# Kernel optimization log

Hardware: AMD Instinct MI355X
Metric: run time of the kernel (lower is better)

## Reference

```python
import jax, jax.numpy as jnp
import numpy as np

# Config: AydinConfig(hidden_dim=1024, intermediate_dim=2048, num_experts=8, top_k=2)
E, H, I, K = 8, 1024, 2048, 2
B, S = 4, 2048


def setup_inputs() -> dict:
    key = jax.random.key(0)
    k1, k2, k3, k4 = jax.random.split(key, 4)
    x = jax.random.normal(k1, (B, S, H), dtype=jnp.float32)
    # nn.Linear(H, E, bias=False): weight shape (E, H), default init ~ U(-1/sqrt(H), 1/sqrt(H))
    router_w = jax.random.uniform(k2, (E, H), dtype=jnp.float32,
                                  minval=-1.0, maxval=1.0) / np.sqrt(H).astype(np.float32)
    # normal init, std=0.02 (reset_parameters)
    w13 = jax.random.normal(k3, (E, H, 2 * I), dtype=jnp.float32) * 0.02
    w2 = jax.random.normal(k4, (E, I, H), dtype=jnp.float32) * 0.02
    return {"x": x, "router_w": router_w, "w13": w13, "w2": w2}


def reference(x, router_w, w13, w2):
    # Router: logits (B,S,E) -> softmax -> top-k with renormalized weights
    logits = jnp.einsum('bsh,eh->bse', x, router_w)
    probs = jax.nn.softmax(logits, axis=-1)
    weights, indices = jax.lax.top_k(probs, K)            # (B,S,K)
    weights = weights / (weights.sum(axis=-1, keepdims=True) + 1e-6)
    # Expert SwiGLU, computed densely over all experts then gathered.
    # Same math as the torch per-token weight gather, but avoids the
    # (B,S,K,H,2I) gathered-weight blowup.
    h13 = jnp.einsum('bsh,ehi->bsei', x, w13)             # (B,S,E,2I)
    gate, up = jnp.split(h13, 2, axis=-1)                 # (B,S,E,I) each
    h = jax.nn.silu(gate) * up
    y = jnp.einsum('bsei,eih->bseh', h, w2)               # (B,S,E,H)
    # Gather top-k expert outputs and combine with routing weights
    y_sel = jnp.take_along_axis(y, indices[..., None], axis=2)  # (B,S,K,H)
    return (y_sel * weights[..., None]).sum(axis=2)       # (B,S,H)
```

## Files before the change

kernel.cpp:

```cpp
#include <hip/hip_runtime.h>
#include <hip/hip_bf16.h>
#include <math.h>

#define NEXP 8
#define HD 1024
#define ID 2048
#define NTOK 8192
#define NROWS 16384

typedef __bf16 bf16_t;
typedef __bf16 bf16x8 __attribute__((ext_vector_type(8)));
typedef float f32x4 __attribute__((ext_vector_type(4)));

#define BK1 64
#define BK2 128
#define MAXT1 72
#define MAXT2 136

__device__ __forceinline__ void gl16(const void* g, void* l) {
    __builtin_amdgcn_global_load_lds(
        (const __attribute__((address_space(1))) unsigned int*)g,
        (__attribute__((address_space(3))) unsigned int*)l, 16, 0, 0);
}

__global__ __launch_bounds__(256)
void router_kernel(const float* __restrict__ x, const float* __restrict__ rw,
                   bf16_t* __restrict__ xb, int* __restrict__ topk_idx,
                   float* __restrict__ topk_w)
{
    const int t = blockIdx.x;
    const int tid = threadIdx.x;
    const float4 xv = ((const float4*)(x + (size_t)t * HD))[tid];
    float acc[NEXP];
#pragma unroll
    for (int e = 0; e < NEXP; ++e) {
        const float4 w4 = ((const float4*)(rw + e * HD))[tid];
        acc[e] = xv.x * w4.x + xv.y * w4.y + xv.z * w4.z + xv.w * w4.w;
    }
    bf16_t tmp[4] = {(bf16_t)xv.x, (bf16_t)xv.y, (bf16_t)xv.z, (bf16_t)xv.w};
    *(uint2*)(xb + (size_t)t * HD + tid * 4) = *(const uint2*)tmp;

    __shared__ float red[4][NEXP];
    const int lane = tid & 63, wv = tid >> 6;
#pragma unroll
    for (int e = 0; e < NEXP; ++e) {
        float v = acc[e];
#pragma unroll
        for (int off = 32; off >= 1; off >>= 1) v += __shfl_down(v, off, 64);
        if (lane == 0) red[wv][e] = v;
    }
    __syncthreads();
    if (tid == 0) {
        float lg[NEXP], mx = -1e30f;
#pragma unroll
        for (int e = 0; e < NEXP; ++e) {
            lg[e] = red[0][e] + red[1][e] + red[2][e] + red[3][e];
            mx = fmaxf(mx, lg[e]);
        }
        float p[NEXP], s = 0.f;
#pragma unroll
        for (int e = 0; e < NEXP; ++e) { p[e] = __expf(lg[e] - mx); s += p[e]; }
        const float inv = 1.f / s;
#pragma unroll
        for (int e = 0; e < NEXP; ++e) p[e] *= inv;
        int i0 = 0; float p0 = p[0];
#pragma unroll
        for (int e = 1; e < NEXP; ++e) if (p[e] > p0) { p0 = p[e]; i0 = e; }
        int i1 = -1; float p1 = -1.f;
#pragma unroll
        for (int e = 0; e < NEXP; ++e) if (e != i0 && p[e] > p1) { p1 = p[e]; i1 = e; }
        const float d = 1.f / (p0 + p1 + 1e-6f);
        topk_idx[t * 2 + 0] = i0; topk_idx[t * 2 + 1] = i1;
        topk_w[t * 2 + 0] = p0 * d; topk_w[t * 2 + 1] = p1 * d;
    }
}

__global__ __launch_bounds__(256)
void count_kernel(const int* __restrict__ topk_idx, int* __restrict__ counts)
{
    __shared__ int lc[NEXP];
    const int tid = threadIdx.x;
    if (tid < NEXP) lc[tid] = 0;
    __syncthreads();
    const int t = blockIdx.x * 256 + tid;
    atomicAdd(&lc[topk_idx[t * 2 + 0]], 1);
    atomicAdd(&lc[topk_idx[t * 2 + 1]], 1);
    __syncthreads();
    if (tid < NEXP) atomicAdd(&counts[tid], lc[tid]);
}

__global__ void scan_kernel(const int* __restrict__ counts, int* __restrict__ offsets,
                            int* __restrict__ cursor,
                            unsigned* __restrict__ map256, unsigned* __restrict__ map128)
{
    __shared__ int tb2[NEXP + 1], tb1[NEXP + 1];
    if (threadIdx.x == 0) {
        int s = 0, t2 = 0, t1 = 0;
        for (int e = 0; e < NEXP; ++e) {
            offsets[e] = s; cursor[e] = s; s += counts[e];
            tb2[e] = t2; t2 += (counts[e] + 255) >> 8;
            tb1[e] = t1; t1 += (counts[e] + 127) >> 7;
        }
        tb2[NEXP] = t2; tb1[NEXP] = t1;
    }
    __syncthreads();
    for (int i = threadIdx.x; i < MAXT1; i += 64) {
        unsigned v = 0xFFFFFFFFu;
#pragma unroll
        for (int e = 0; e < NEXP; ++e)
            if (i >= tb2[e] && i < tb2[e + 1]) v = ((unsigned)e << 16) | (unsigned)(i - tb2[e]);
        map256[i] = v;
    }
    for (int i = threadIdx.x; i < MAXT2; i += 64) {
        unsigned v = 0xFFFFFFFFu;
#pragma unroll
        for (int e = 0; e < NEXP; ++e)
            if (i >= tb1[e] && i < tb1[e + 1]) v = ((unsigned)e << 16) | (unsigned)(i - tb1[e]);
        map128[i] = v;
    }
}

__global__ __launch_bounds__(256)
void scatter_kernel(const int* __restrict__ topk_idx, const float* __restrict__ topk_w,
                    int* __restrict__ cursor, int* __restrict__ token_list,
                    float* __restrict__ row_w, int* __restrict__ row_pos)
{
    __shared__ int lc[NEXP], gbase[NEXP];
    const int tid = threadIdx.x;
    if (tid < NEXP) lc[tid] = 0;
    __syncthreads();
    const int t = blockIdx.x * 256 + tid;
    const int e0 = topk_idx[t * 2 + 0], e1 = topk_idx[t * 2 + 1];
    const int lp0 = atomicAdd(&lc[e0], 1);
    const int lp1 = atomicAdd(&lc[e1], 1);
    __syncthreads();
    if (tid < NEXP) gbase[tid] = atomicAdd(&cursor[tid], lc[tid]);
    __syncthreads();
    const int p0 = gbase[e0] + lp0, p1 = gbase[e1] + lp1;
    token_list[p0] = t; row_w[p0] = topk_w[t * 2 + 0]; row_pos[t * 2 + 0] = p0;
    token_list[p1] = t; row_w[p1] = topk_w[t * 2 + 1]; row_pos[t * 2 + 1] = p1;
}

__global__ __launch_bounds__(256)
void precast_kernel(const float* __restrict__ src, bf16_t* __restrict__ dst,
                    int K, int N)
{
    const int e = blockIdx.z;
    src += (size_t)e * K * N;
    dst += (size_t)e * K * N;
    const int n0 = blockIdx.x * 64, k0 = blockIdx.y * 64;
    __shared__ float tile[64][65];
    const int tid = threadIdx.x;
    const int tx = (tid & 15) * 4, ty = tid >> 4;
#pragma unroll
    for (int p = 0; p < 4; ++p) {
        const float4 v = *(const float4*)(src + (size_t)(k0 + ty + p * 16) * N + n0 + tx);
        tile[ty + p * 16][tx + 0] = v.x;
        tile[ty + p * 16][tx + 1] = v.y;
        tile[ty + p * 16][tx + 2] = v.z;
        tile[ty + p * 16][tx + 3] = v.w;
    }
    __syncthreads();
    const int n = tid >> 2, kc = (tid & 3) * 16;
    bf16_t outv[16];
#pragma unroll
    for (int j = 0; j < 16; ++j) outv[j] = (bf16_t)tile[kc + j][n];
    bf16_t* d = dst + (size_t)(n0 + n) * K + k0 + kc;
    *(uint4*)d = *(uint4*)outv;
    *(uint4*)(d + 8) = *((uint4*)outv + 1);
}

__global__ __launch_bounds__(512)
void gemm1_kernel(const bf16_t* __restrict__ xb, const bf16_t* __restrict__ w13b,
                  const int* __restrict__ offsets, const int* __restrict__ counts,
                  const int* __restrict__ token_list,
                  const unsigned* __restrict__ tile_map, bf16_t* __restrict__ hbuf)
{
    unsigned id = blockIdx.y * 32u + blockIdx.x;
    id = (id & 7u) * 288u + (id >> 3);
    const unsigned tm = tile_map[id >> 5];
    if (tm == 0xFFFFFFFFu) return;
    const int e = (int)(tm >> 16), mt = (int)(tm & 0xFFFFu);
    const int rows = counts[e];
    const int row_base = offsets[e];
    const int r0 = mt * 256;
    const int n0 = (int)(id & 31u) * 64;

    __shared__ alignas(16) bf16_t As[256][64];
    __shared__ alignas(16) bf16_t Bg[64][64];
    __shared__ alignas(16) bf16_t Bu[64][64];

    const int tid = threadIdx.x;
    const int lane = tid & 63;
    const int wv = tid >> 6;
    const int wr = wv >> 1, wc = wv & 1;
    const int ln15 = lane & 15, q = lane >> 4;
    const int x7 = ln15 & 7;
    const int c0 = ((q ^ x7)) * 8;
    const int c1 = c0 ^ 32;

    const int srow = tid >> 3;
    const int scol = ((tid & 7) ^ ((tid >> 3) & 7)) * 8;
    const bf16_t* ap[4];
#pragma unroll
    for (int p = 0; p < 4; ++p) {
        int gr = row_base + r0 + p * 64 + srow;
        if (gr > NROWS - 1) gr = NROWS - 1;
        ap[p] = xb + (size_t)token_list[gr] * HD + scol;
    }
    const bf16_t* wb = w13b + (size_t)e * HD * (2 * ID);
    const bf16_t* bgp = wb + (size_t)(n0 + srow) * HD + scol;
    const bf16_t* bup = wb + (size_t)(ID + n0 + srow) * HD + scol;
    bf16_t* const d_bg = &Bg[0][0] + tid * 8;
    bf16_t* const d_bu = &Bu[0][0] + tid * 8;

    f32x4 accG[4][2], accU[4][2];
#pragma unroll
    for (int i = 0; i < 4; ++i)
#pragma unroll
        for (int j = 0; j < 2; ++j)
#pragma unroll
            for (int c = 0; c < 4; ++c) { accG[i][j][c] = 0.f; accU[i][j][c] = 0.f; }

    for (int k0 = 0; k0 < HD; k0 += BK1) {
#pragma unroll
        for (int p = 0; p < 4; ++p) {
            gl16(ap[p], &As[0][0] + (p * 512 + tid) * 8);
            ap[p] += BK1;
        }
        gl16(bgp, d_bg); gl16(bup, d_bu);
        bgp += BK1; bup += BK1;
        __syncthreads();

#pragma unroll
        for (int kk = 0; kk < 2; ++kk) {
            const int cc = kk ? c1 : c0;
            bf16x8 af[4], bgf[2], buf_[2];
#pragma unroll
            for (int i = 0; i < 4; ++i)
                af[i] = *(const bf16x8*)&As[wr * 64 + i * 16 + ln15][cc];
#pragma unroll
            for (int j = 0; j < 2; ++j) {
                bgf[j]  = *(const bf16x8*)&Bg[wc * 32 + j * 16 + ln15][cc];
                buf_[j] = *(const bf16x8*)&Bu[wc * 32 + j * 16 + ln15][cc];
            }
#pragma unroll
            for (int i = 0; i < 4; ++i)
#pragma unroll
                for (int j = 0; j < 2; ++j) {
                    accG[i][j] = __builtin_amdgcn_mfma_f32_16x16x32_bf16(af[i], bgf[j], accG[i][j], 0, 0, 0);
                    accU[i][j] = __builtin_amdgcn_mfma_f32_16x16x32_bf16(af[i], buf_[j], accU[i][j], 0, 0, 0);
                }
        }
        __syncthreads();
    }

#pragma unroll
    for (int i = 0; i < 4; ++i) {
#pragma unroll
        for (int reg = 0; reg < 4; ++reg) {
            const int rr = wr * 64 + i * 16 + q * 4 + reg;
            if (r0 + rr < rows) {
                bf16_t* dst = hbuf + (size_t)(row_base + r0 + rr) * ID + n0 + wc * 32 + ln15;
#pragma unroll
                for (int j = 0; j < 2; ++j) {
                    const float g = accG[i][j][reg], u = accU[i][j][reg];
                    dst[j * 16] = (bf16_t)((g / (1.f + __expf(-g))) * u);
                }
            }
        }
    }
}

__global__ __launch_bounds__(512)
void gemm2_kernel(const bf16_t* __restrict__ hbuf, const bf16_t* __restrict__ w2b,
                  const int* __restrict__ offsets, const int* __restrict__ counts,
                  const float* __restrict__ row_w,
                  const unsigned* __restrict__ tile_map, float* __restrict__ ybuf)
{
    const unsigned tm = tile_map[blockIdx.y];
    if (tm == 0xFFFFFFFFu) return;
    const int e = (int)(tm >> 16), mt = (int)(tm & 0xFFFFu);
    const int rows = counts[e];
    const int row_base = offsets[e];
    const int r0 = mt * 128;
    const int n0 = blockIdx.x * 128;

    __shared__ alignas(16) bf16_t As[128][128];
    __shared__ alignas(16) bf16_t Bs[128][128];
    __shared__ float rww_s[128];

    const int tid = threadIdx.x;
    if (tid < 128) {
        int gr = row_base + r0 + tid; if (gr > NROWS - 1) gr = NROWS - 1;
        rww_s[tid] = row_w[gr];
    }
    const int lane = tid & 63;
    const int wv = tid >> 6;
    const int wr = wv >> 1, wc = wv & 1;
    const int ln15 = lane & 15, q = lane >> 4;

    const int srow = tid >> 4;
    const int scol = ((tid & 15) ^ ((tid >> 4) & 15)) * 8;
    const bf16_t* ap[4];
    const bf16_t* bp[4];
    const bf16_t* w2e = w2b + (size_t)e * ID * HD;
#pragma unroll
    for (int p = 0; p < 4; ++p) {
        int gr = row_base + r0 + p * 32 + srow;
        if (gr > NROWS - 1) gr = NROWS - 1;
        ap[p] = hbuf + (size_t)gr * ID + scol;
        bp[p] = w2e + (size_t)(n0 + p * 32 + srow) * ID + scol;
    }

    f32x4 acc[2][4];
#pragma unroll
    for (int i = 0; i < 2; ++i)
#pragma unroll
        for (int j = 0; j < 4; ++j)
#pragma unroll
            for (int c = 0; c < 4; ++c) acc[i][j][c] = 0.f;

    for (int k0 = 0; k0 < ID; k0 += BK2) {
#pragma unroll
        for (int p = 0; p < 4; ++p) {
            gl16(ap[p], &As[0][0] + (p * 512 + tid) * 8);
            gl16(bp[p], &Bs[0][0] + (p * 512 + tid) * 8);
            ap[p] += BK2; bp[p] += BK2;
        }
        __syncthreads();

#pragma unroll
        for (int kk = 0; kk < 4; ++kk) {
            const int cc = ((kk * 4 + q) ^ ln15) * 8;
            bf16x8 af[2], bf_[4];
#pragma unroll
            for (int i = 0; i < 2; ++i)
                af[i] = *(const bf16x8*)&As[wr * 32 + i * 16 + ln15][cc];
#pragma unroll
            for (int j = 0; j < 4; ++j)
                bf_[j] = *(const bf16x8*)&Bs[wc * 64 + j * 16 + ln15][cc];
#pragma unroll
            for (int i = 0; i < 2; ++i)
#pragma unroll
                for (int j = 0; j < 4; ++j)
                    acc[i][j] = __builtin_amdgcn_mfma_f32_16x16x32_bf16(af[i], bf_[j], acc[i][j], 0, 0, 0);
        }
        __syncthreads();
    }

#pragma unroll
    for (int i = 0; i < 2; ++i) {
#pragma unroll
        for (int reg = 0; reg < 4; ++reg) {
            const int rr = wr * 32 + i * 16 + q * 4 + reg;
            if (r0 + rr < rows) {
                const float w = rww_s[rr];
                float* dst = ybuf + (size_t)(row_base + r0 + rr) * HD + n0 + wc * 64 + ln15;
#pragma unroll
                for (int j = 0; j < 4; ++j)
                    dst[j * 16] = acc[i][j][reg] * w;
            }
        }
    }
}

__global__ __launch_bounds__(256)
void combine_kernel(const float* __restrict__ ybuf, const int* __restrict__ row_pos,
                    float* __restrict__ out)
{
    const int t = blockIdx.x;
    const int p0 = row_pos[t * 2 + 0], p1 = row_pos[t * 2 + 1];
    const float4 a = ((const float4*)(ybuf + (size_t)p0 * HD))[threadIdx.x];
    const float4 b = ((const float4*)(ybuf + (size_t)p1 * HD))[threadIdx.x];
    float4 o; o.x = a.x + b.x; o.y = a.y + b.y; o.z = a.z + b.z; o.w = a.w + b.w;
    ((float4*)(out + (size_t)t * HD))[threadIdx.x] = o;
}

extern "C" void kernel_launch(void* const* d_in, const int* in_sizes, int n_in,
                              void* d_out, int out_size, void* d_ws, size_t ws_size,
                              hipStream_t stream) {
    const float* x   = (const float*)d_in[0];
    const float* rw  = (const float*)d_in[1];
    const float* w13 = (const float*)d_in[2];
    const float* w2  = (const float*)d_in[3];
    float* out = (float*)d_out;

    char* ws = (char*)d_ws;
    int*      counts     = (int*)(ws + 0);
    int*      cursor     = (int*)(ws + 64);
    int*      offsets    = (int*)(ws + 128);
    int*      topk_idx   = (int*)(ws + 256);
    float*    topk_w     = (float*)(ws + 256 + 1 * 65536);
    int*      token_list = (int*)(ws + 256 + 2 * 65536);
    float*    row_w      = (float*)(ws + 256 + 3 * 65536);
    int*      row_pos    = (int*)(ws + 256 + 4 * 65536);
    unsigned* map256     = (unsigned*)(ws + 256 + 5 * 65536);
    unsigned* map128     = (unsigned*)(ws + 256 + 6 * 65536);
    const size_t MB = 1024 * 1024;
    bf16_t* xb   = (bf16_t*)(ws + 1 * MB);
    bf16_t* hbuf = (bf16_t*)(ws + 17 * MB);
    bf16_t* w13b = (bf16_t*)(ws + 81 * MB);
    float*  ybuf = (float*)(ws + 81 * MB);
    bf16_t* w2b  = (bf16_t*)(ws + 145 * MB);

    hipMemsetAsync(ws, 0, 256, stream);

    dim3 gp1(2 * ID / 64, HD / 64, NEXP);
    precast_kernel<<<gp1, 256, 0, stream>>>(w13, w13b, HD, 2 * ID);
    dim3 gp2(HD / 64, ID / 64, NEXP);
    precast_kernel<<<gp2, 256, 0, stream>>>(w2, w2b, ID, HD);

    router_kernel<<<NTOK, 256, 0, stream>>>(x, rw, xb, topk_idx, topk_w);
    count_kernel<<<NTOK / 256, 256, 0, stream>>>(topk_idx, counts);
    scan_kernel<<<1, 64, 0, stream>>>(counts, offsets, cursor, map256, map128);
    scatter_kernel<<<NTOK / 256, 256, 0, stream>>>(topk_idx, topk_w, cursor,
                                                   token_list, row_w, row_pos);

    dim3 g1(ID / 64, MAXT1);
    gemm1_kernel<<<g1, 512, 0, stream>>>(xb, w13b, offsets, counts, token_list,
                                         map256, hbuf);
    dim3 g2(HD / 128, MAXT2);
    gemm2_kernel<<<g2, 512, 0, stream>>>(hbuf, w2b, offsets, counts, row_w,
                                         map128, ybuf);
    combine_kernel<<<NTOK, 256, 0, stream>>>(ybuf, row_pos, out);
}
```

Before: 566.6 us.

## Triple-buffer gemm1 LDS with async prefetch and swizzle gemm2 block order

Replaces gemm1's single-buffered 64-wide K loop, which synchronised twice per step, with a three-slot LDS ring of 32-wide K tiles. The next tile's global-to-LDS loads are issued before computing the current one, using a manual vmcnt wait and a single barrier per step, so memory latency overlaps with MFMA work. It also remaps gemm2 block IDs so the 8 N-tiles sharing an expert tile are spread across XCDs, matching the remapping gemm1 already uses. The trade-offs are more LDS per block, which may lower occupancy, and hand-tuned waitcnt logic that is fragile if the load count per stage changes.

Result: no change. 566.4 us (-0.0%).

```diff
diff --git a/kernel.cpp b/kernel.cpp
--- a/kernel.cpp
+++ b/kernel.cpp
@@ -12,10 +12,11 @@
 typedef __bf16 bf16x8 __attribute__((ext_vector_type(8)));
 typedef float f32x4 __attribute__((ext_vector_type(4)));
 
-#define BK1 64
+#define BK1 32
 #define BK2 128
 #define MAXT1 72
 #define MAXT2 136
+#define SLOT1 12288
 
 __device__ __forceinline__ void gl16(const void* g, void* l) {
     __builtin_amdgcn_global_load_lds(
@@ -186,33 +187,27 @@
     const int r0 = mt * 256;
     const int n0 = (int)(id & 31u) * 64;
 
-    __shared__ alignas(16) bf16_t As[256][64];
-    __shared__ alignas(16) bf16_t Bg[64][64];
-    __shared__ alignas(16) bf16_t Bu[64][64];
+    __shared__ alignas(16) bf16_t lds1[3 * SLOT1];
 
     const int tid = threadIdx.x;
     const int lane = tid & 63;
     const int wv = tid >> 6;
     const int wr = wv >> 1, wc = wv & 1;
     const int ln15 = lane & 15, q = lane >> 4;
-    const int x7 = ln15 & 7;
-    const int c0 = ((q ^ x7)) * 8;
-    const int c1 = c0 ^ 32;
-
-    const int srow = tid >> 3;
-    const int scol = ((tid & 7) ^ ((tid >> 3) & 7)) * 8;
-    const bf16_t* ap[4];
-#pragma unroll
-    for (int p = 0; p < 4; ++p) {
-        int gr = row_base + r0 + p * 64 + srow;
-        if (gr > NROWS - 1) gr = NROWS - 1;
-        ap[p] = xb + (size_t)token_list[gr] * HD + scol;
-    }
+    const int cs = (q ^ ((ln15 >> 1) & 3)) * 8;
+
+    const int srowA = tid >> 2;
+    const int scol = ((tid & 3) ^ ((tid >> 3) & 3)) * 8;
+    const int tb = tid & 255;
+    const int srowB = tb >> 2;
+    const int scolB = ((tb & 3) ^ ((tb >> 3) & 3)) * 8;
+    int grA0 = row_base + r0 + srowA;       if (grA0 > NROWS - 1) grA0 = NROWS - 1;
+    int grA1 = row_base + r0 + 128 + srowA; if (grA1 > NROWS - 1) grA1 = NROWS - 1;
+    const bf16_t* ap0 = xb + (size_t)token_list[grA0] * HD + scol;
+    const bf16_t* ap1 = xb + (size_t)token_list[grA1] * HD + scol;
     const bf16_t* wb = w13b + (size_t)e * HD * (2 * ID);
-    const bf16_t* bgp = wb + (size_t)(n0 + srow) * HD + scol;
-    const bf16_t* bup = wb + (size_t)(ID + n0 + srow) * HD + scol;
-    bf16_t* const d_bg = &Bg[0][0] + tid * 8;
-    bf16_t* const d_bu = &Bu[0][0] + tid * 8;
+    const bf16_t* bp0 = wb + (size_t)((tid < 256 ? 0 : ID) + n0 + srowB) * HD + scolB;
+    const int boff = (tid < 256 ? 8192 : 10240) + tb * 8;
 
     f32x4 accG[4][2], accU[4][2];
 #pragma unroll
@@ -222,38 +217,55 @@
 #pragma unroll
             for (int c = 0; c < 4; ++c) { accG[i][j][c] = 0.f; accU[i][j][c] = 0.f; }
 
-    for (int k0 = 0; k0 < HD; k0 += BK1) {
-#pragma unroll
-        for (int p = 0; p < 4; ++p) {
-            gl16(ap[p], &As[0][0] + (p * 512 + tid) * 8);
-            ap[p] += BK1;
-        }
-        gl16(bgp, d_bg); gl16(bup, d_bu);
-        bgp += BK1; bup += BK1;
-        __syncthreads();
-
-#pragma unroll
-        for (int kk = 0; kk < 2; ++kk) {
-            const int cc = kk ? c1 : c0;
-            bf16x8 af[4], bgf[2], buf_[2];
-#pragma unroll
-            for (int i = 0; i < 4; ++i)
-                af[i] = *(const bf16x8*)&As[wr * 64 + i * 16 + ln15][cc];
-#pragma unroll
-            for (int j = 0; j < 2; ++j) {
-                bgf[j]  = *(const bf16x8*)&Bg[wc * 32 + j * 16 + ln15][cc];
-                buf_[j] = *(const bf16x8*)&Bu[wc * 32 + j * 16 + ln15][cc];
-            }
-#pragma unroll
-            for (int i = 0; i < 4; ++i)
-#pragma unroll
-                for (int j = 0; j < 2; ++j) {
-                    accG[i][j] = __builtin_amdgcn_mfma_f32_16x16x32_bf16(af[i], bgf[j], accG[i][j], 0, 0, 0);
-                    accU[i][j] = __builtin_amdgcn_mfma_f32_16x16x32_bf16(af[i], buf_[j], accU[i][j], 0, 0, 0);
-                }
-        }
-        __syncthreads();
-    }
+#define G1_STG(SB, KT) do { \
+    const int kk_ = (KT) * BK1; \
+    gl16(ap0 + kk_, lds1 + (SB) + tid * 8); \
+    gl16(ap1 + kk_, lds1 + (SB) + 4096 + tid * 8); \
+    gl16(bp0 + kk_, lds1 + (SB) + boff); \
+} while (0)
+
+#define G1_COMP(SB) do { \
+    const bf16_t* A_  = lds1 + (SB); \
+    const bf16_t* BG_ = lds1 + (SB) + 8192; \
+    const bf16_t* BU_ = lds1 + (SB) + 10240; \
+    bf16x8 af[4], bgf[2], buf_[2]; \
+    _Pragma("unroll") \
+    for (int i_ = 0; i_ < 4; ++i_) \
+        af[i_] = *(const bf16x8*)&A_[(wr * 64 + i_ * 16 + ln15) * 32 + cs]; \
+    _Pragma("unroll") \
+    for (int j_ = 0; j_ < 2; ++j_) { \
+        bgf[j_]  = *(const bf16x8*)&BG_[(wc * 32 + j_ * 16 + ln15) * 32 + cs]; \
+        buf_[j_] = *(const bf16x8*)&BU_[(wc * 32 + j_ * 16 + ln15) * 32 + cs]; \
+    } \
+    _Pragma("unroll") \
+    for (int i_ = 0; i_ < 4; ++i_) \
+        _Pragma("unroll") \
+        for (int j_ = 0; j_ < 2; ++j_) { \
+            accG[i_][j_] = __builtin_amdgcn_mfma_f32_16x16x32_bf16(af[i_], bgf[j_], accG[i_][j_], 0, 0, 0); \
+            accU[i_][j_] = __builtin_amdgcn_mfma_f32_16x16x32_bf16(af[i_], buf_[j_], accU[i_][j_], 0, 0, 0); \
+        } \
+} while (0)
+
+    asm volatile("" :: "s"(rows), "s"(row_base));
+    asm volatile("" :: "v"(ap0), "v"(ap1), "v"(bp0));
+    asm volatile("s_waitcnt vmcnt(0)" ::: "memory");
+
+    G1_STG(0, 0);
+    int sc = 0, ss = SLOT1;
+    for (int t = 0; t < 31; ++t) {
+        G1_STG(ss, t + 1);
+        asm volatile("s_waitcnt vmcnt(3)" ::: "memory");
+        __builtin_amdgcn_s_barrier();
+        __builtin_amdgcn_sched_barrier(0);
+        G1_COMP(sc);
+        sc = ss; ss += SLOT1; if (ss == 3 * SLOT1) ss = 0;
+    }
+    asm volatile("s_waitcnt vmcnt(0)" ::: "memory");
+    __builtin_amdgcn_s_barrier();
+    __builtin_amdgcn_sched_barrier(0);
+    G1_COMP(sc);
+#undef G1_STG
+#undef G1_COMP
 
 #pragma unroll
     for (int i = 0; i < 4; ++i) {
@@ -278,13 +290,15 @@
                   const float* __restrict__ row_w,
                   const unsigned* __restrict__ tile_map, float* __restrict__ ybuf)
 {
-    const unsigned tm = tile_map[blockIdx.y];
+    unsigned id = blockIdx.y * 8u + blockIdx.x;
+    id = (id & 7u) * 136u + (id >> 3);
+    const unsigned tm = tile_map[id >> 3];
     if (tm == 0xFFFFFFFFu) return;
     const int e = (int)(tm >> 16), mt = (int)(tm & 0xFFFFu);
     const int rows = counts[e];
     const int row_base = offsets[e];
     const int r0 = mt * 128;
-    const int n0 = blockIdx.x * 128;
+    const int n0 = (int)(id & 7u) * 128;
 
     __shared__ alignas(16) bf16_t As[128][128];
     __shared__ alignas(16) bf16_t Bs[128][128];
```
